# Optimization experiments

Measured on AMD Instinct MI355X. Metric: run time of the kernel, lower is better.

Reference implementation:

```python
import jax, jax.numpy as jnp
import numpy as np

RADIUS = 0.2
K = 32  # num_neighbors


def setup_inputs() -> dict:
    key = jax.random.key(0)
    k1, k2, k3 = jax.random.split(key, 3)
    points_xyz = jax.random.uniform(k1, (2, 16384, 3), dtype=jnp.float32)
    center_xyz = jax.random.uniform(k2, (2, 2048, 3), dtype=jnp.float32)
    features = jax.random.normal(k3, (2, 64, 16384), dtype=jnp.float32)
    return {"points_xyz": points_xyz, "center_xyz": center_xyz, "features": features}


def _ball_query(center_xyz, points_xyz, k, radius):
    # squared distances (B, G, N) via ||c||^2 + ||p||^2 - 2 c.p (avoids (B,G,N,3) temp)
    c2 = jnp.sum(center_xyz * center_xyz, axis=-1)  # (B, G)
    p2 = jnp.sum(points_xyz * points_xyz, axis=-1)  # (B, N)
    cp = jnp.einsum('bgd,bnd->bgn', center_xyz, points_xyz)
    d2 = c2[:, :, None] + p2[:, None, :] - 2.0 * cp  # (B, G, N)
    n = points_xyz.shape[1]
    # key = point index if inside ball else sentinel N; first-K-in-ball == K smallest keys
    keys = jnp.where(d2 < radius * radius, jnp.arange(n, dtype=jnp.int32), n)
    neg_vals, _ = jax.lax.top_k(-keys, k)
    idx = -neg_vals  # (B, G, K) ascending point indices, sentinel n if <k found
    first = idx[..., :1]
    # pad missing slots with first found index (CUDA ball_query semantics), 0 if none
    idx = jnp.where(idx < n, idx, jnp.where(first < n, first, 0))
    return idx


def reference(points_xyz, center_xyz, features):
    idx = _ball_query(center_xyz, points_xyz, K, RADIUS)  # (B, G, K) int32
    gather = jax.vmap(lambda f, i: f[:, i])  # (C, N), (G, K) -> (C, G, K)
    grouped_xyz = gather(jnp.swapaxes(points_xyz, 1, 2), idx)  # (B, 3, G, K)
    # relative_xyz then normalize_xyz
    grouped_xyz = (grouped_xyz - jnp.swapaxes(center_xyz, 1, 2)[..., None]) / RADIUS
    grouped_features = gather(features, idx)  # (B, C, G, K)
    return grouped_xyz, grouped_features
```

## Files before the change

### kernel.cpp

```cpp
#include <hip/hip_runtime.h>
#include <hip/hip_bf16.h>

constexpr int NPTS = 16384;
constexpr int NCTR = 2048;
constexpr int NCH  = 64;
constexpr int KK   = 32;
constexpr int NB   = 2;
#define R2 0.04f

__global__ __launch_bounds__(256) void prep_kernel(
    const float* __restrict__ points,
    const float* __restrict__ feats,
    float* __restrict__ featsT,
    float4* __restrict__ packed)
{
#pragma clang fp contract(off)
    __shared__ float tile[64][65];

    if (blockIdx.x < 512) {
        const int b  = blockIdx.x >> 8;
        const int n0 = (blockIdx.x & 255) * 64;
        const int t  = threadIdx.x;
        const int nl = t & 63;
        const int q  = t >> 6;

        const float* fb = feats + (size_t)b * NCH * NPTS;
#pragma unroll
        for (int r = 0; r < 16; ++r) {
            int c = r * 4 + q;
            tile[c][nl] = fb[(size_t)c * NPTS + n0 + nl];
        }
        __syncthreads();
        float* ftb = featsT + ((size_t)b * NPTS + n0) * NCH;
#pragma unroll
        for (int r = 0; r < 16; ++r) {
            int n = r * 4 + q;
            ftb[(size_t)n * NCH + nl] = tile[nl][n];
        }
        return;
    }

    const int tid = (blockIdx.x - 512) * 256 + threadIdx.x;
#pragma unroll
    for (int s = 0; s < 4; ++s) {
        const int i = tid + s * 8192;
        const float x = points[3 * i + 0];
        const float y = points[3 * i + 1];
        const float z = points[3 * i + 2];
        const float p2 = (x * x + y * y) + z * z;
        packed[i] = make_float4(x, y, z, p2);
    }
}

__global__ __launch_bounds__(256, 4) void query_group(
    const float4* __restrict__ packed,
    const float* __restrict__ centers,
    const float* __restrict__ featsT,
    float* __restrict__ out_xyz,
    float* __restrict__ out_feat)
{
#pragma clang fp contract(off)
    __shared__ int   s_idx[4][KK];
    __shared__ float s_f[4][KK][68];

    const int wave = threadIdx.x >> 6;
    const int lane = threadIdx.x & 63;
    const int cg   = blockIdx.x * 4 + wave;
    const int b    = cg >> 11;
    const int g    = cg & (NCTR - 1);

    const float4* pk = packed + (size_t)b * NPTS;
    const float* cc = centers + (size_t)cg * 3;
    const float cx = cc[0], cy = cc[1], cz = cc[2];
    const float c2 = (cx * cx + cy * cy) + cz * cz;

    int* idxs = s_idx[wave];

    float4 cur[8], nxt[8];
#pragma unroll
    for (int j = 0; j < 8; ++j) cur[j] = pk[j * 64 + lane];
    int cnt = 0;
    for (int base = 0; base < NPTS; base += 512) {
        const int nbb = (base + 512 < NPTS) ? base + 512 : 0;
#pragma unroll
        for (int j = 0; j < 8; ++j) nxt[j] = pk[nbb + j * 64 + lane];
#pragma unroll
        for (int j = 0; j < 8; ++j) {
            const float4 v = cur[j];
            const float cp = (cx * v.x + cy * v.y) + cz * v.z;
            const float d2 = (c2 + v.w) - 2.0f * cp;
            const bool hit = d2 < R2;
            const unsigned long long m = __ballot(hit);
            if (hit) {
                const int slot = cnt + __popcll(m & ((1ull << lane) - 1ull));
                if (slot < KK) idxs[slot] = base + j * 64 + lane;
            }
            cnt += (int)__popcll(m);
        }
        if (cnt >= KK) break;
#pragma unroll
        for (int j = 0; j < 8; ++j) cur[j] = nxt[j];
    }
    __syncthreads();

    const int cpd = cnt < KK ? cnt : KK;
    const int first = (cnt > 0) ? idxs[0] : 0;
    if (lane < KK) {
        const int id = (lane < cpd) ? idxs[lane] : first;
        idxs[lane] = id;
        const float4 v = pk[id];
        const size_t ob = (((size_t)b * 3 + 0) * NCTR + g) * KK + lane;
        out_xyz[ob + (size_t)0 * NCTR * KK] = (v.x - cx) / 0.2f;
        out_xyz[ob + (size_t)1 * NCTR * KK] = (v.y - cy) / 0.2f;
        out_xyz[ob + (size_t)2 * NCTR * KK] = (v.z - cz) / 0.2f;
    }
    __syncthreads();

    float (*sf)[68] = s_f[wave];
    const int li = lane & 15, r = lane >> 4;
    const float* ftb = featsT + (size_t)b * NPTS * NCH;
#pragma unroll
    for (int i = 0; i < 8; ++i) {
        const int k = i * 4 + r;
        const float4 v = *((const float4*)(ftb + (size_t)idxs[k] * NCH) + li);
        *(float4*)&sf[k][4 * li] = v;
    }
    __syncthreads();

    const int kq = lane & 7;
    const int c0 = lane >> 3;
    const size_t ob = ((size_t)b * NCH * NCTR + g) * KK;
#pragma unroll
    for (int p = 0; p < 8; ++p) {
        const int c = c0 + 8 * p;
        float4 v;
        v.x = sf[4 * kq + 0][c];
        v.y = sf[4 * kq + 1][c];
        v.z = sf[4 * kq + 2][c];
        v.w = sf[4 * kq + 3][c];
        *(float4*)(out_feat + ob + (size_t)c * NCTR * KK + 4 * kq) = v;
    }
}

__global__ __launch_bounds__(256) void ballquery_group(
    const float* __restrict__ points, const float* __restrict__ centers,
    const float* __restrict__ feats, float* __restrict__ out_xyz,
    float* __restrict__ out_feat)
{
#pragma clang fp contract(off)
    __shared__ int   s_idx[4][KK];
    __shared__ float s_f[4][KK][65];
    const int wave = threadIdx.x >> 6, lane = threadIdx.x & 63;
    const int cg = blockIdx.x * 4 + wave;
    const int b = cg >> 11, g = cg & (NCTR - 1);
    const float* pb = points + (size_t)b * NPTS * 3;
    const float* cc = centers + (size_t)cg * 3;
    const float cx = cc[0], cy = cc[1], cz = cc[2];
    const float c2 = (cx * cx + cy * cy) + cz * cz;
    int* idxs = s_idx[wave];
    int cnt = 0;
    for (int base = 0; base < NPTS; base += 64) {
        const int i = base + lane;
        const float px = pb[i * 3 + 0], py = pb[i * 3 + 1], pz = pb[i * 3 + 2];
        const float p2 = (px * px + py * py) + pz * pz;
        const float cp = (cx * px + cy * py) + cz * pz;
        const float d2 = (c2 + p2) - 2.0f * cp;
        const bool hit = d2 < R2;
        const unsigned long long m = __ballot(hit);
        if (hit) {
            const int slot = cnt + __popcll(m & ((1ull << lane) - 1ull));
            if (slot < KK) idxs[slot] = i;
        }
        cnt += (int)__popcll(m);
        if (cnt >= KK) break;
    }
    __syncthreads();
    const int cpd = cnt < KK ? cnt : KK;
    const int first = (cnt > 0) ? idxs[0] : 0;
    if (lane < KK) idxs[lane] = (lane < cpd) ? idxs[lane] : first;
    __syncthreads();
    if (lane < KK) {
        const int id = idxs[lane];
        const float px = pb[id * 3 + 0], py = pb[id * 3 + 1], pz = pb[id * 3 + 2];
        const size_t ob = (((size_t)b * 3 + 0) * NCTR + g) * KK + lane;
        out_xyz[ob + (size_t)0 * NCTR * KK] = (px - cx) / 0.2f;
        out_xyz[ob + (size_t)1 * NCTR * KK] = (py - cy) / 0.2f;
        out_xyz[ob + (size_t)2 * NCTR * KK] = (pz - cz) / 0.2f;
    }
    float (*sf)[65] = s_f[wave];
    const float* fb = feats + (size_t)b * NCH * NPTS;
    for (int k = 0; k < KK; ++k) {
        const int id = idxs[k];
        sf[k][lane] = fb[(size_t)lane * NPTS + id];
    }
    __syncthreads();
    const int k = lane & 31, ch = lane >> 5;
    const size_t ob = ((size_t)b * NCH * NCTR + g) * KK;
#pragma unroll
    for (int cc2 = 0; cc2 < 32; ++cc2) {
        const int c = cc2 * 2 + ch;
        out_feat[ob + (size_t)c * NCTR * KK + k] = sf[k][c];
    }
}

extern "C" void kernel_launch(void* const* d_in, const int* in_sizes, int n_in,
                              void* d_out, int out_size, void* d_ws, size_t ws_size,
                              hipStream_t stream) {
    const float* points  = (const float*)d_in[0];
    const float* centers = (const float*)d_in[1];
    const float* feats   = (const float*)d_in[2];

    float* out      = (float*)d_out;
    float* out_xyz  = out;
    float* out_feat = out + (size_t)NB * 3 * NCTR * KK;

    const size_t ftBytes = (size_t)NB * NPTS * NCH * sizeof(float);
    const size_t pkBytes = (size_t)NB * NPTS * 4 * sizeof(float);

    if (ws_size >= ftBytes + pkBytes) {
        float*  featsT = (float*)d_ws;
        float4* packed = (float4*)((char*)d_ws + ftBytes);
        prep_kernel<<<544, 256, 0, stream>>>(points, feats, featsT, packed);
        query_group<<<(NB * NCTR) / 4, 256, 0, stream>>>(
            packed, centers, featsT, out_xyz, out_feat);
    } else {
        ballquery_group<<<(NB * NCTR) / 4, 256, 0, stream>>>(
            points, centers, feats, out_xyz, out_feat);
    }
}
```

Before: 86.23 us.

## Split each center's ball query across four waves of a block

Each block now handles one center instead of four, and its four waves scan interleaved 512-point slices of a 2048-point chunk in parallel. Per-wave hit counts are merged through shared memory with a prefix sum so the first-K-in-order semantics are kept. The aim is to shorten the serial scan latency per center and to raise the number of blocks from 1024 to 4096. In exchange it adds two block-wide barriers per chunk and may scan up to 2047 extra points past the K-th hit. The launch-bounds occupancy hint is also dropped.

```diff
diff --git a/kernel.cpp b/kernel.cpp
--- a/kernel.cpp
+++ b/kernel.cpp
@@ -52,7 +52,7 @@
     }
 }
 
-__global__ __launch_bounds__(256, 4) void query_group(
+__global__ __launch_bounds__(256) void query_group(
     const float4* __restrict__ packed,
     const float* __restrict__ centers,
     const float* __restrict__ featsT,
@@ -60,12 +60,14 @@
     float* __restrict__ out_feat)
 {
 #pragma clang fp contract(off)
-    __shared__ int   s_idx[4][KK];
-    __shared__ float s_f[4][KK][68];
+    __shared__ int   lidx[4][KK];
+    __shared__ int   scnt[4];
+    __shared__ int   idxs[KK];
+    __shared__ float sf[KK][68];
 
     const int wave = threadIdx.x >> 6;
     const int lane = threadIdx.x & 63;
-    const int cg   = blockIdx.x * 4 + wave;
+    const int cg   = blockIdx.x;
     const int b    = cg >> 11;
     const int g    = cg & (NCTR - 1);
 
@@ -74,16 +76,18 @@
     const float cx = cc[0], cy = cc[1], cz = cc[2];
     const float c2 = (cx * cx + cy * cy) + cz * cz;
 
-    int* idxs = s_idx[wave];
-
+    const int off0 = wave * 512 + lane;
     float4 cur[8], nxt[8];
 #pragma unroll
-    for (int j = 0; j < 8; ++j) cur[j] = pk[j * 64 + lane];
-    int cnt = 0;
-    for (int base = 0; base < NPTS; base += 512) {
-        const int nbb = (base + 512 < NPTS) ? base + 512 : 0;
-#pragma unroll
-        for (int j = 0; j < 8; ++j) nxt[j] = pk[nbb + j * 64 + lane];
+    for (int j = 0; j < 8; ++j) cur[j] = pk[off0 + j * 64];
+
+    int gcnt = 0;
+    for (int base = 0; base < NPTS; base += 2048) {
+        const int nbb = (base + 2048 < NPTS) ? base + 2048 : 0;
+#pragma unroll
+        for (int j = 0; j < 8; ++j) nxt[j] = pk[nbb + off0 + j * 64];
+
+        int lc = 0;
 #pragma unroll
         for (int j = 0; j < 8; ++j) {
             const float4 v = cur[j];
@@ -92,47 +96,63 @@
             const bool hit = d2 < R2;
             const unsigned long long m = __ballot(hit);
             if (hit) {
-                const int slot = cnt + __popcll(m & ((1ull << lane) - 1ull));
-                if (slot < KK) idxs[slot] = base + j * 64 + lane;
+                const int slot = lc + __popcll(m & ((1ull << lane) - 1ull));
+                if (slot < KK) lidx[wave][slot] = base + off0 + j * 64;
             }
-            cnt += (int)__popcll(m);
-        }
-        if (cnt >= KK) break;
+            lc += (int)__popcll(m);
+        }
+        if (lane == 0) scnt[wave] = lc;
+        __syncthreads();
+
+        int pre = 0, tot = 0;
+#pragma unroll
+        for (int w = 0; w < 4; ++w) {
+            const int c = scnt[w];
+            tot += c;
+            if (w < wave) pre += c;
+        }
+        const int nl = lc < KK ? lc : KK;
+        if (lane < nl) {
+            const int gs = gcnt + pre + lane;
+            if (gs < KK) idxs[gs] = lidx[wave][lane];
+        }
+        gcnt += tot;
+        __syncthreads();
+        if (gcnt >= KK) break;
 #pragma unroll
         for (int j = 0; j < 8; ++j) cur[j] = nxt[j];
     }
     __syncthreads();
 
-    const int cpd = cnt < KK ? cnt : KK;
-    const int first = (cnt > 0) ? idxs[0] : 0;
-    if (lane < KK) {
-        const int id = (lane < cpd) ? idxs[lane] : first;
-        idxs[lane] = id;
+    const int cpd = gcnt < KK ? gcnt : KK;
+    const int first = (gcnt > 0) ? idxs[0] : 0;
+    if (threadIdx.x < KK) {
+        const int id = (threadIdx.x < cpd) ? idxs[threadIdx.x] : first;
+        idxs[threadIdx.x] = id;
         const float4 v = pk[id];
-        const size_t ob = (((size_t)b * 3 + 0) * NCTR + g) * KK + lane;
+        const size_t ob = (((size_t)b * 3 + 0) * NCTR + g) * KK + threadIdx.x;
         out_xyz[ob + (size_t)0 * NCTR * KK] = (v.x - cx) / 0.2f;
         out_xyz[ob + (size_t)1 * NCTR * KK] = (v.y - cy) / 0.2f;
         out_xyz[ob + (size_t)2 * NCTR * KK] = (v.z - cz) / 0.2f;
     }
     __syncthreads();
 
-    float (*sf)[68] = s_f[wave];
     const int li = lane & 15, r = lane >> 4;
     const float* ftb = featsT + (size_t)b * NPTS * NCH;
 #pragma unroll
-    for (int i = 0; i < 8; ++i) {
-        const int k = i * 4 + r;
+    for (int i = 0; i < 2; ++i) {
+        const int k = wave * 8 + i * 4 + r;
         const float4 v = *((const float4*)(ftb + (size_t)idxs[k] * NCH) + li);
         *(float4*)&sf[k][4 * li] = v;
     }
     __syncthreads();
 
-    const int kq = lane & 7;
-    const int c0 = lane >> 3;
+    const int kq = threadIdx.x & 7;
+    const int c0 = threadIdx.x >> 3;
     const size_t ob = ((size_t)b * NCH * NCTR + g) * KK;
 #pragma unroll
-    for (int p = 0; p < 8; ++p) {
-        const int c = c0 + 8 * p;
+    for (int p = 0; p < 2; ++p) {
+        const int c = c0 + 32 * p;
         float4 v;
         v.x = sf[4 * kq + 0][c];
         v.y = sf[4 * kq + 1][c];
@@ -221,7 +241,7 @@
         float*  featsT = (float*)d_ws;
         float4* packed = (float4*)((char*)d_ws + ftBytes);
         prep_kernel<<<544, 256, 0, stream>>>(points, feats, featsT, packed);
-        query_group<<<(NB * NCTR) / 4, 256, 0, stream>>>(
+        query_group<<<NB * NCTR, 256, 0, stream>>>(
             packed, centers, featsT, out_xyz, out_feat);
     } else {
         ballquery_group<<<(NB * NCTR) / 4, 256, 0, stream>>>(
```

New measurement: 88.29 us. 1.02x slower.
